# Performance work log

Measured on AMD Instinct MI355X. Metric: run time of the kernel, lower is better.

The kernel has to match this reference:

```python
import jax, jax.numpy as jnp
import numpy as np

G = 512      # graphs per batch
NPG = 64     # nodes per graph (EEG channels)
N = G * NPG  # total nodes = 32768
DEG = 32     # avg degree
E = N * DEG  # total edges = 1048576
F_IN, F1, F2, F3, K = 64, 128, 128, 64, 3


def setup_inputs() -> dict:
    key = jax.random.key(0)
    ks = jax.random.split(key, 8)
    rng = np.random.default_rng(0)
    # block-wise random edges: every edge stays inside its 64-node graph
    base = np.repeat(np.arange(G, dtype=np.int64) * NPG, NPG * DEG)
    row = jnp.asarray(base + rng.integers(0, NPG, E))
    col = jnp.asarray(base + rng.integers(0, NPG, E))
    batch = jnp.asarray(np.repeat(np.arange(G, dtype=np.int64), NPG))
    x = jax.random.normal(ks[0], (N, F_IN), jnp.float32)
    edge_weight = jax.random.uniform(ks[1], (E,), jnp.float32, 0.1, 1.0)

    def xav(k, shape):
        lim = (6.0 / (shape[-2] + shape[-1])) ** 0.5
        return jax.random.uniform(k, shape, jnp.float32, -lim, lim)

    return {
        'x': x, 'edge_weight': edge_weight,
        'W1': xav(ks[2], (K, F_IN, F1)), 'b1': jnp.zeros((F1,), jnp.float32),
        'W2': xav(ks[3], (K, F1, F2)),  'b2': jnp.zeros((F2,), jnp.float32),
        'W3': xav(ks[4], (K, F2, F3)),  'b3': jnp.zeros((F3,), jnp.float32),
        'fc_w': xav(ks[5], (2 * F3, F3)), 'fc_b': jnp.zeros((F3,), jnp.float32),
        'row': row, 'col': col, 'batch': batch,
    }


def cheb_conv(x, row, col, ew, W, b):
    # PyG ChebConv with sym normalization, lambda_max = 2:
    # L_hat = 2L/lambda_max - I = -D^{-1/2} A D^{-1/2}  (diagonal is exactly 0)
    deg = jax.ops.segment_sum(ew, row, num_segments=N)
    safe = jnp.where(deg > 0, deg, 1.0)
    dinv = jnp.where(deg > 0, jax.lax.rsqrt(safe), 0.0)
    nw = -(dinv[row] * ew * dinv[col])  # off-diagonal entries of L_hat

    def prop(t):  # t: [N, F] -> L_hat @ t via gather-scale-scatter
        return jax.ops.segment_sum(nw[:, None] * t[row], col, num_segments=N)

    Tx0 = x
    out = Tx0 @ W[0]
    Tx1 = prop(Tx0)
    out = out + Tx1 @ W[1]
    for k in range(2, K):  # Chebyshev recursion T_k = 2 L_hat T_{k-1} - T_{k-2}
        Tx2 = 2.0 * prop(Tx1) - Tx0
        out = out + Tx2 @ W[k]
        Tx0, Tx1 = Tx1, Tx2
    return out + b


def reference(x, edge_weight, W1, b1, W2, b2, W3, b3, fc_w, fc_b, row, col, batch):
    h = jax.nn.relu(cheb_conv(x, row, col, edge_weight, W1, b1))
    h = jax.nn.relu(cheb_conv(h, row, col, edge_weight, W2, b2))
    h = cheb_conv(h, row, col, edge_weight, W3, b3)
    # meanmax readout over graphs
    counts = jax.ops.segment_sum(jnp.ones((N,), h.dtype), batch, num_segments=G)
    h_mean = jax.ops.segment_sum(h, batch, num_segments=G) / counts[:, None]
    h_max = jax.ops.segment_max(h, batch, num_segments=G)
    pooled = jnp.concatenate([h_mean, h_max], axis=1)  # [G, 2*F3]
    return pooled @ fc_w + fc_b
```

## Files before the change

### kernel.cpp

```cpp
#include <hip/hip_runtime.h>
#include <hip/hip_bf16.h>
#include <math.h>

typedef float  f32x4  __attribute__((ext_vector_type(4)));
typedef short  bf16x8 __attribute__((ext_vector_type(8)));

#define NG  512
#define EPG 2048

#define B1_OFF 0
#define B2_OFF 16384
#define B3_OFF 32768
#define B4_OFF 49152
#define B5_OFF 65536
#define LDS_SZ 81920
#define SASTR  65

static __device__ __forceinline__ unsigned short f2bf(float f) {
    union { __hip_bfloat16 b; unsigned short u; } c;
    c.b = __float2bfloat16(f);
    return c.u;
}
static __device__ __forceinline__ float bf2f(unsigned short h) {
    union { unsigned u; float f; } v; v.u = ((unsigned)h) << 16;
    return v.f;
}
static __device__ __forceinline__ unsigned pk2(float lo, float hi) {
    return (unsigned)f2bf(lo) | ((unsigned)f2bf(hi) << 16);
}
static __device__ __forceinline__ bf16x8 ubf(uint4 u) {
    union { uint4 a; bf16x8 b; } c; c.a = u; return c.b;
}

__global__ __launch_bounds__(64) void wpack(
    const float* __restrict__ W1, const float* __restrict__ W2,
    const float* __restrict__ W3, uint4* __restrict__ Wp)
{
    int b = blockIdx.x, lane = threadIdx.x;
    const float* W; int FIN, FOUT, rel, off;
    if (b < 48)       { W = W1; FIN = 64;  FOUT = 128; rel = b;       off = 0;   }
    else if (b < 144) { W = W2; FIN = 128; FOUT = 128; rel = b - 48;  off = 48;  }
    else              { W = W3; FIN = 128; FOUT = 64;  rel = b - 144; off = 144; }
    int NKT = FIN / 32, NNT = FOUT / 16;
    int sl = rel / (NKT * NNT), r2 = rel % (NKT * NNT);
    int kt = r2 / NNT, nt = r2 % NNT;
    int lg = lane >> 4, li = lane & 15;
    int fin0 = kt*32 + lg*8, fout = nt*16 + li;
    unsigned v[4];
#pragma unroll
    for (int jp = 0; jp < 4; ++jp) {
        float a0, a1;
#pragma unroll
        for (int h = 0; h < 2; ++h) {
            const size_t base = (size_t)(fin0 + 2*jp + h) * FOUT + fout;
            const float w0  = W[base];
            const float w1v = W[(size_t)FIN*FOUT + base];
            const float w2v = W[(size_t)2*FIN*FOUT + base];
            const float val = (sl == 0) ? w0 : (sl == 1) ? w2v : (w1v - w0);
            if (h == 0) a0 = val; else a1 = val;
        }
        v[jp] = pk2(a0, a1);
    }
    Wp[(size_t)(off + rel)*64 + lane] = make_uint4(v[0],v[1],v[2],v[3]);
}

template <int FIN, int FOUT, bool RELU, bool LAST>
static __device__ __forceinline__ void layer(
    char* smem, const uint4* __restrict__ Wp, const float* __restrict__ bias,
    int w, int lg, int li, int lane)
{
    constexpr int NKT = FIN / 32;
    constexpr int NNT = FOUT / 16;
    constexpr int NFO = FOUT / 32;
    constexpr int TST = FIN * 2;
    constexpr int TSM = (FIN == 128) ? 15 : 7;

    char* Ht = smem + B1_OFF;
    char* V1 = smem + B2_OFF;
    char* V2 = smem + B3_OFF;
    char* V3 = smem + B4_OFF;
    const char* Ln  = smem + B5_OFF;
    const char* L2n = smem + B5_OFF + 8192;

    {
        const int mt  = (FIN == 128) ? w : (w & 3);
        const int nt0 = (FIN == 128) ? 0 : ((w >> 2) * 2);
        constexpr int NTN = (FIN == 128) ? 4 : 2;
        const int frow = mt * 16 + li;
        const int fsw  = (frow & 7) << 4;
        bf16x8 a[2];
#pragma unroll
        for (int kt = 0; kt < 2; ++kt)
            a[kt] = *(const bf16x8*)(Ht + frow*128 + ((kt*64 + lg*16) ^ fsw));
        const int fb = mt * 16 + lg * 4;
#pragma unroll
        for (int j = 0; j < NTN; ++j) {
            const int nrow = (nt0 + j) * 16 + li;
            const int lsw  = (nrow & 7) << 4;
            f32x4 p2 = {0.f,0.f,0.f,0.f}, p3 = {0.f,0.f,0.f,0.f};
#pragma unroll
            for (int kt = 0; kt < 2; ++kt) {
                uint4 bL  = *(const uint4*)(Ln  + nrow*128 + ((kt*64 + lg*16) ^ lsw));
                uint4 bL2 = *(const uint4*)(L2n + nrow*128 + ((kt*64 + lg*16) ^ lsw));
                p3 = __builtin_amdgcn_mfma_f32_16x16x32_bf16(a[kt], ubf(bL),  p3, 0,0,0);
                p2 = __builtin_amdgcn_mfma_f32_16x16x32_bf16(a[kt], ubf(bL2), p2, 0,0,0);
            }
            float t0v[4];
#pragma unroll
            for (int r = 0; r < 4; ++r)
                t0v[r] = bf2f(*(const unsigned short*)(
                    Ht + (fb + r)*128 + ((nrow*2) ^ (((fb + r) & 7) << 4))));
            const int cb = (fb * 2) ^ ((nrow & TSM) << 4);
            *(uint2*)(V1 + nrow*TST + cb) =
                make_uint2(pk2(p3[0]+t0v[0], p3[1]+t0v[1]), pk2(p3[2]+t0v[2], p3[3]+t0v[3]));
            *(uint2*)(V2 + nrow*TST + cb) = make_uint2(pk2(p2[0],p2[1]), pk2(p2[2],p2[3]));
            *(uint2*)(V3 + nrow*TST + cb) = make_uint2(pk2(p3[0],p3[1]), pk2(p3[2],p3[3]));
        }
    }
    __syncthreads();

    const int mw = w & 3, foh = w >> 2;
    f32x4 acc[NFO];
#pragma unroll
    for (int i = 0; i < NFO; ++i) acc[i] = (f32x4){0.f,0.f,0.f,0.f};
    {
        const int arow = mw * 16 + li;
        const int asw  = (arow & TSM) << 4;
#pragma unroll
        for (int sl = 0; sl < 3; ++sl) {
            const char* src = (sl == 0) ? V1 : (sl == 1) ? V2 : V3;
#pragma unroll
            for (int k = 0; k < NKT; ++k) {
                bf16x8 ta = *(const bf16x8*)(src + arow*TST + ((k*64 + lg*16) ^ asw));
#pragma unroll
                for (int fi = 0; fi < NFO; ++fi) {
                    uint4 wf = Wp[((size_t)(sl*NKT + k)*NNT + foh*NFO + fi)*64 + lane];
                    acc[fi] = __builtin_amdgcn_mfma_f32_16x16x32_bf16(ta, ubf(wf), acc[fi], 0,0,0);
                }
            }
        }
    }
    if (!LAST) {
#pragma unroll
        for (int fi = 0; fi < NFO; ++fi) {
            const int fo = (foh*NFO + fi)*16 + li;
            const float bv = bias[fo];
            f32x4 v = acc[fi];
            float o0 = v[0]+bv, o1 = v[1]+bv, o2 = v[2]+bv, o3 = v[3]+bv;
            if (RELU) { o0=fmaxf(o0,0.f); o1=fmaxf(o1,0.f); o2=fmaxf(o2,0.f); o3=fmaxf(o3,0.f); }
            const int node0 = mw*16 + lg*4;
            *(uint2*)(smem + B1_OFF + fo*128 + ((node0*2) ^ ((fo & 7) << 4))) =
                make_uint2(pk2(o0,o1), pk2(o2,o3));
        }
    } else {
        float* pS = (float*)(smem + B5_OFF + 8192);
        float* pM = pS + 256;
#pragma unroll
        for (int fi = 0; fi < NFO; ++fi) {
            const int fo = (foh*NFO + fi)*16 + li;
            f32x4 v = acc[fi];
            float s = v[0]+v[1]+v[2]+v[3];
            float m = fmaxf(fmaxf(v[0],v[1]), fmaxf(v[2],v[3]));
            s += __shfl_xor(s, 16); s += __shfl_xor(s, 32);
            m = fmaxf(m, __shfl_xor(m, 16)); m = fmaxf(m, __shfl_xor(m, 32));
            if (lg == 0) { pS[mw*64 + fo] = s; pM[mw*64 + fo] = m; }
        }
    }
    __syncthreads();
}

__global__ __launch_bounds__(512, 4) void fused(
    const float* __restrict__ X,  const float* __restrict__ ew,
    const int* __restrict__ row,  const int* __restrict__ col,
    const uint4* __restrict__ Wp,
    const float* __restrict__ b1, const float* __restrict__ b2,
    const float* __restrict__ b3,
    const float* __restrict__ fcw, const float* __restrict__ fcb,
    float* __restrict__ outp)
{
    __shared__ __align__(16) char smem[LDS_SZ];
    const int g = blockIdx.x, t = threadIdx.x;
    const int w = t >> 6, lane = t & 63, lg = lane >> 4, li = lane & 15;

    const float4* xg = (const float4*)(X + (size_t)g * 4096);
    float4 xv0 = xg[t], xv1 = xg[t + 512];
    const int e0 = g * EPG;
    int er[4], ec[4]; float ev[4];
#pragma unroll
    for (int j = 0; j < 4; ++j) {
        er[j] = row[e0 + t + 512*j] & 63;
        ec[j] = col[e0 + t + 512*j] & 63;
        ev[j] = ew[e0 + t + 512*j];
    }

    float* sAT  = (float*)(smem + B2_OFF);
    float* sdeg = (float*)(smem + B4_OFF);

    for (int i = t; i < 64 * SASTR; i += 512) sAT[i] = 0.f;
    if (t < 64) sdeg[t] = 0.f;
    __syncthreads();
#pragma unroll
    for (int j = 0; j < 4; ++j) {
        atomicAdd(&sAT[ec[j]*SASTR + er[j]], ev[j]);
        atomicAdd(&sdeg[er[j]], ev[j]);
    }
    __syncthreads();
    {
        const int n = t >> 3, k0 = (t & 7) * 8;
        const float dsn = sdeg[n];
        const float dn = dsn > 0.f ? rsqrtf(dsn) : 0.f;
        float vv[8];
#pragma unroll
        for (int j = 0; j < 8; ++j) {
            const float dk0 = sdeg[k0 + j];
            const float dk = dk0 > 0.f ? rsqrtf(dk0) : 0.f;
            const float v = -sAT[n*SASTR + k0 + j] * dk * dn;
            sAT[n*SASTR + k0 + j] = v;
            vv[j] = v;
        }
        *(uint4*)(smem + B5_OFF + n*128 + ((k0*2) ^ ((n & 7) << 4))) =
            make_uint4(pk2(vv[0],vv[1]), pk2(vv[2],vv[3]), pk2(vv[4],vv[5]), pk2(vv[6],vv[7]));
#pragma unroll
        for (int half = 0; half < 2; ++half) {
            const int i = t + half * 512;
            const float4 v = half ? xv1 : xv0;
            const int node = i >> 4, f0 = (i & 15) * 4;
            unsigned short h[4] = { f2bf(v.x), f2bf(v.y), f2bf(v.z), f2bf(v.w) };
#pragma unroll
            for (int r = 0; r < 4; ++r)
                *(unsigned short*)(smem + B1_OFF + (f0+r)*128 +
                                   ((node*2) ^ (((f0+r) & 7) << 4))) = h[r];
        }
    }
    __syncthreads();
    {
        const int mt2 = w & 3, nth = w >> 2;
        const int k1 = mt2*16 + li;
        bf16x8 a2[2];
#pragma unroll
        for (int kt = 0; kt < 2; ++kt) {
            float av[8];
#pragma unroll
            for (int j = 0; j < 8; ++j)
                av[j] = sAT[(kt*32 + lg*8 + j)*SASTR + k1];
            union { uint4 u; bf16x8 b; } c;
            c.u = make_uint4(pk2(av[0],av[1]), pk2(av[2],av[3]),
                             pk2(av[4],av[5]), pk2(av[6],av[7]));
            a2[kt] = c.b;
        }
#pragma unroll
        for (int j = 0; j < 2; ++j) {
            const int nrow = (nth*2 + j)*16 + li;
            const int lsw  = (nrow & 7) << 4;
            f32x4 p = {0.f,0.f,0.f,0.f};
#pragma unroll
            for (int kt = 0; kt < 2; ++kt) {
                uint4 bf = *(const uint4*)(smem + B5_OFF + nrow*128 + ((kt*64 + lg*16) ^ lsw));
                p = __builtin_amdgcn_mfma_f32_16x16x32_bf16(a2[kt], ubf(bf), p, 0,0,0);
            }
            unsigned short q[4];
#pragma unroll
            for (int r = 0; r < 4; ++r) {
                const int kk = mt2*16 + lg*4 + r;
                q[r] = f2bf(2.f*p[r] - ((kk == nrow) ? 1.f : 0.f));
            }
            *(uint2*)(smem + B5_OFF + 8192 + nrow*128 + (((mt2*16 + lg*4)*2) ^ lsw)) =
                make_uint2(q[0] | ((unsigned)q[1] << 16), q[2] | ((unsigned)q[3] << 16));
        }
    }
    __syncthreads();

    layer<64, 128, true,  false>(smem, Wp,                  b1, w, lg, li, lane);
    layer<128, 128, true, false>(smem, Wp + (size_t)48*64,  b2, w, lg, li, lane);
    layer<128, 64, false, true >(smem, Wp + (size_t)144*64, b3, w, lg, li, lane);

    float* pS   = (float*)(smem + B5_OFF + 8192);
    float* pM   = pS + 256;
    float* sme  = (float*)(smem + B3_OFF);
    float* smx  = sme + 64;
    float* part = smx + 64;
    if (t < 64) {
        float s = pS[t] + pS[64+t] + pS[128+t] + pS[192+t];
        float m = fmaxf(fmaxf(pM[t], pM[64+t]), fmaxf(pM[128+t], pM[192+t]));
        sme[t] = s * (1.f/64.f) + b3[t];
        smx[t] = m + b3[t];
    }
    __syncthreads();
    if (t < 128) {
        const int j = t & 63, h = t >> 6;
        const float* wv = fcw + (size_t)h*64*64;
        const float* sv = h ? smx : sme;
        float a = 0.f;
        for (int f2 = 0; f2 < 64; ++f2) a += sv[f2] * wv[f2*64 + j];
        part[t] = a;
    }
    __syncthreads();
    if (t < 64) outp[(size_t)g*64 + t] = part[t] + part[64 + t] + fcb[t];
}

extern "C" void kernel_launch(void* const* d_in, const int* in_sizes, int n_in,
                              void* d_out, int out_size, void* d_ws, size_t ws_size,
                              hipStream_t stream)
{
    const float* x   = (const float*)d_in[0];
    const float* ew  = (const float*)d_in[1];
    const float* W1  = (const float*)d_in[2];
    const float* b1  = (const float*)d_in[3];
    const float* W2  = (const float*)d_in[4];
    const float* b2  = (const float*)d_in[5];
    const float* W3  = (const float*)d_in[6];
    const float* b3  = (const float*)d_in[7];
    const float* fcw = (const float*)d_in[8];
    const float* fcb = (const float*)d_in[9];
    const int*   row = (const int*)d_in[10];
    const int*   col = (const int*)d_in[11];

    uint4* Wp = (uint4*)d_ws;

    wpack<<<192, 64, 0, stream>>>(W1, W2, W3, Wp);
    fused<<<NG, 512, 0, stream>>>(x, ew, row, col, Wp,
                                  b1, b2, b3, fcw, fcb, (float*)d_out);
}
```

Baseline: 40.87 us.

## Keep normalized Laplacian operand fragments in registers across all three layers

The bf16 L_hat and 2L_hat^2 - I operand fragments are now loaded once into per-thread registers (aL, aL2) and reused by every layer's propagation MFMAs, instead of being re-read from LDS in each layer. This removes the separate bf16 Ln buffer and shrinks LDS from 80 KB to 72 KB, which could allow more resident blocks per CU. The final FC readout is also spread over all 512 threads with an 8-way partial-sum reduction instead of 128 threads doing 64-long dot products. The trade-off is 16 extra uint4 registers per thread, which adds register pressure under the 512x4 launch bound.

```diff
diff --git a/kernel.cpp b/kernel.cpp
--- a/kernel.cpp
+++ b/kernel.cpp
@@ -8,13 +8,13 @@
 #define NG  512
 #define EPG 2048
 
-#define B1_OFF 0
-#define B2_OFF 16384
-#define B3_OFF 32768
-#define B4_OFF 49152
-#define B5_OFF 65536
-#define LDS_SZ 81920
-#define SASTR  65
+#define B1_OFF  0
+#define V1_OFF  16384
+#define V2_OFF  32768
+#define V3_OFF  49152
+#define L2N_OFF 65536
+#define LDS_SZ  73728
+#define SASTR   66
 
 static __device__ __forceinline__ unsigned short f2bf(float f) {
     union { __hip_bfloat16 b; unsigned short u; } c;
@@ -66,7 +66,8 @@
 
 template <int FIN, int FOUT, bool RELU, bool LAST>
 static __device__ __forceinline__ void layer(
-    char* smem, const uint4* __restrict__ Wp, const float* __restrict__ bias,
+    char* smem, const uint4 (&aL)[2][4], const uint4 (&aL2)[2][4],
+    const uint4* __restrict__ Wp, const float* __restrict__ bias,
     int w, int lg, int li, int lane)
 {
     constexpr int NKT = FIN / 32;
@@ -76,11 +77,9 @@
     constexpr int TSM = (FIN == 128) ? 15 : 7;
 
     char* Ht = smem + B1_OFF;
-    char* V1 = smem + B2_OFF;
-    char* V2 = smem + B3_OFF;
-    char* V3 = smem + B4_OFF;
-    const char* Ln  = smem + B5_OFF;
-    const char* L2n = smem + B5_OFF + 8192;
+    char* V1 = smem + V1_OFF;
+    char* V2 = smem + V2_OFF;
+    char* V3 = smem + V3_OFF;
 
     {
         const int mt  = (FIN == 128) ? w : (w & 3);
@@ -95,15 +94,13 @@
         const int fb = mt * 16 + lg * 4;
 #pragma unroll
         for (int j = 0; j < NTN; ++j) {
-            const int nrow = (nt0 + j) * 16 + li;
-            const int lsw  = (nrow & 7) << 4;
+            const int nt   = nt0 + j;
+            const int nrow = nt * 16 + li;
             f32x4 p2 = {0.f,0.f,0.f,0.f}, p3 = {0.f,0.f,0.f,0.f};
 #pragma unroll
             for (int kt = 0; kt < 2; ++kt) {
-                uint4 bL  = *(const uint4*)(Ln  + nrow*128 + ((kt*64 + lg*16) ^ lsw));
-                uint4 bL2 = *(const uint4*)(L2n + nrow*128 + ((kt*64 + lg*16) ^ lsw));
-                p3 = __builtin_amdgcn_mfma_f32_16x16x32_bf16(a[kt], ubf(bL),  p3, 0,0,0);
-                p2 = __builtin_amdgcn_mfma_f32_16x16x32_bf16(a[kt], ubf(bL2), p2, 0,0,0);
+                p3 = __builtin_amdgcn_mfma_f32_16x16x32_bf16(a[kt], ubf(aL[kt][nt]),  p3, 0,0,0);
+                p2 = __builtin_amdgcn_mfma_f32_16x16x32_bf16(a[kt], ubf(aL2[kt][nt]), p2, 0,0,0);
             }
             float t0v[4];
 #pragma unroll
@@ -153,7 +150,7 @@
                 make_uint2(pk2(o0,o1), pk2(o2,o3));
         }
     } else {
-        float* pS = (float*)(smem + B5_OFF + 8192);
+        float* pS = (float*)(smem + L2N_OFF);
         float* pM = pS + 256;
 #pragma unroll
         for (int fi = 0; fi < NFO; ++fi) {
@@ -193,8 +190,8 @@
         ev[j] = ew[e0 + t + 512*j];
     }
 
-    float* sAT  = (float*)(smem + B2_OFF);
-    float* sdeg = (float*)(smem + B4_OFF);
+    float* sAT  = (float*)(smem + V1_OFF);
+    float* sdeg = (float*)(smem + L2N_OFF);
 
     for (int i = t; i < 64 * SASTR; i += 512) sAT[i] = 0.f;
     if (t < 64) sdeg[t] = 0.f;
@@ -209,17 +206,12 @@
         const int n = t >> 3, k0 = (t & 7) * 8;
         const float dsn = sdeg[n];
         const float dn = dsn > 0.f ? rsqrtf(dsn) : 0.f;
-        float vv[8];
 #pragma unroll
         for (int j = 0; j < 8; ++j) {
             const float dk0 = sdeg[k0 + j];
             const float dk = dk0 > 0.f ? rsqrtf(dk0) : 0.f;
-            const float v = -sAT[n*SASTR + k0 + j] * dk * dn;
-            sAT[n*SASTR + k0 + j] = v;
-            vv[j] = v;
-        }
-        *(uint4*)(smem + B5_OFF + n*128 + ((k0*2) ^ ((n & 7) << 4))) =
-            make_uint4(pk2(vv[0],vv[1]), pk2(vv[2],vv[3]), pk2(vv[4],vv[5]), pk2(vv[6],vv[7]));
+            sAT[n*SASTR + k0 + j] = -sAT[n*SASTR + k0 + j] * dk * dn;
+        }
 #pragma unroll
         for (int half = 0; half < 2; ++half) {
             const int i = t + half * 512;
@@ -233,6 +225,17 @@
         }
     }
     __syncthreads();
+
+    uint4 aL[2][4];
+#pragma unroll
+    for (int kt = 0; kt < 2; ++kt)
+#pragma unroll
+        for (int nt = 0; nt < 4; ++nt) {
+            const float* rp = &sAT[(nt*16 + li)*SASTR + kt*32 + lg*8];
+            float a0 = rp[0], a1 = rp[1], a2_ = rp[2], a3 = rp[3];
+            float a4 = rp[4], a5 = rp[5], a6 = rp[6], a7 = rp[7];
+            aL[kt][nt] = make_uint4(pk2(a0,a1), pk2(a2_,a3), pk2(a4,a5), pk2(a6,a7));
+        }
     {
         const int mt2 = w & 3, nth = w >> 2;
         const int k1 = mt2*16 + li;
@@ -250,35 +253,44 @@
         }
 #pragma unroll
         for (int j = 0; j < 2; ++j) {
-            const int nrow = (nth*2 + j)*16 + li;
+            const int nt   = nth*2 + j;
+            const int nrow = nt*16 + li;
             const int lsw  = (nrow & 7) << 4;
             f32x4 p = {0.f,0.f,0.f,0.f};
 #pragma unroll
-            for (int kt = 0; kt < 2; ++kt) {
-                uint4 bf = *(const uint4*)(smem + B5_OFF + nrow*128 + ((kt*64 + lg*16) ^ lsw));
-                p = __builtin_amdgcn_mfma_f32_16x16x32_bf16(a2[kt], ubf(bf), p, 0,0,0);
-            }
+            for (int kt = 0; kt < 2; ++kt)
+                p = __builtin_amdgcn_mfma_f32_16x16x32_bf16(a2[kt], ubf(aL[kt][nt]), p, 0,0,0);
             unsigned short q[4];
 #pragma unroll
             for (int r = 0; r < 4; ++r) {
                 const int kk = mt2*16 + lg*4 + r;
                 q[r] = f2bf(2.f*p[r] - ((kk == nrow) ? 1.f : 0.f));
             }
-            *(uint2*)(smem + B5_OFF + 8192 + nrow*128 + (((mt2*16 + lg*4)*2) ^ lsw)) =
+            *(uint2*)(smem + L2N_OFF + nrow*128 + (((mt2*16 + lg*4)*2) ^ lsw)) =
                 make_uint2(q[0] | ((unsigned)q[1] << 16), q[2] | ((unsigned)q[3] << 16));
         }
     }
     __syncthreads();
 
-    layer<64, 128, true,  false>(smem, Wp,                  b1, w, lg, li, lane);
-    layer<128, 128, true, false>(smem, Wp + (size_t)48*64,  b2, w, lg, li, lane);
-    layer<128, 64, false, true >(smem, Wp + (size_t)144*64, b3, w, lg, li, lane);
-
-    float* pS   = (float*)(smem + B5_OFF + 8192);
-    float* pM   = pS + 256;
-    float* sme  = (float*)(smem + B3_OFF);
-    float* smx  = sme + 64;
-    float* part = smx + 64;
+    uint4 aL2[2][4];
+#pragma unroll
+    for (int kt = 0; kt < 2; ++kt)
+#pragma unroll
+        for (int nt = 0; nt < 4; ++nt) {
+            const int nrow = nt*16 + li;
+            const int lsw  = (nrow & 7) << 4;
+            aL2[kt][nt] = *(const uint4*)(smem + L2N_OFF + nrow*128 + ((kt*64 + lg*16) ^ lsw));
+        }
+
+    layer<64, 128, true,  false>(smem, aL, aL2, Wp,                  b1, w, lg, li, lane);
+    layer<128, 128, true, false>(smem, aL, aL2, Wp + (size_t)48*64,  b2, w, lg, li, lane);
+    layer<128, 64, false, true >(smem, aL, aL2, Wp + (size_t)144*64, b3, w, lg, li, lane);
+
+    float* pS    = (float*)(smem + L2N_OFF);
+    float* pM    = pS + 256;
+    float* sme   = pM + 256;
+    float* smx   = sme + 64;
+    float* part8 = (float*)(smem + V1_OFF);
     if (t < 64) {
         float s = pS[t] + pS[64+t] + pS[128+t] + pS[192+t];
         float m = fmaxf(fmaxf(pM[t], pM[64+t]), fmaxf(pM[128+t], pM[192+t]));
@@ -286,16 +298,24 @@
         smx[t] = m + b3[t];
     }
     __syncthreads();
-    if (t < 128) {
-        const int j = t & 63, h = t >> 6;
+    {
+        const int j = t & 63, q = t >> 6;
+        const int h = q >> 2, s = q & 3;
         const float* wv = fcw + (size_t)h*64*64;
         const float* sv = h ? smx : sme;
         float a = 0.f;
-        for (int f2 = 0; f2 < 64; ++f2) a += sv[f2] * wv[f2*64 + j];
-        part[t] = a;
-    }
-    __syncthreads();
-    if (t < 64) outp[(size_t)g*64 + t] = part[t] + part[64 + t] + fcb[t];
+#pragma unroll
+        for (int f2 = s*16; f2 < s*16 + 16; ++f2)
+            a += sv[f2] * wv[f2*64 + j];
+        part8[q*64 + j] = a;
+    }
+    __syncthreads();
+    if (t < 64) {
+        float a = fcb[t];
+#pragma unroll
+        for (int q = 0; q < 8; ++q) a += part8[q*64 + t];
+        outp[(size_t)g*64 + t] = a;
+    }
 }
 
 extern "C" void kernel_launch(void* const* d_in, const int* in_sizes, int n_in,
```

After: 70.76 us. +73.1%, slower.
